# Performance work log

Hardware: AMD Instinct MI355X
Metric: run time of the kernel (lower is better)

The kernel has to match this reference:

```python
import jax, jax.numpy as jnp
import numpy as np

T, H, F = 4096, 4096, 14336

def setup_inputs() -> dict:
    key = jax.random.key(0)
    k1, k2, k3, k4 = jax.random.split(key, 4)
    s = 1.0 / np.sqrt(H)
    return {
        "x": jax.random.normal(k1, (T, H), dtype=jnp.float32),
        "expert_w1": jax.random.normal(k2, (H, F), dtype=jnp.float32) * s,
        "expert_v1": jax.random.normal(k3, (H, F), dtype=jnp.float32) * s,
        "expert_w2": jax.random.normal(k4, (H, F), dtype=jnp.float32) * s,
    }

def reference(x, expert_w1, expert_v1, expert_w2):
    # SwiGLU expert FFN: silu(x @ w1) * (x @ v1) @ w2.T
    gate_proj = jax.nn.silu(x @ expert_w1)          # [T, F]
    up_proj = x @ expert_v1                          # [T, F]
    down_proj = (gate_proj * up_proj) @ expert_w2.T  # [T, H]
    return down_proj
```

## Files before the change

kernel.cpp:

```cpp
#include <hip/hip_runtime.h>
#include <hip/hip_bf16.h>
#include <stdint.h>

#define TT 4096
#define HH 4096
#define FF 14336
#define NCAT (2 * FF)

typedef __attribute__((ext_vector_type(8))) short bf16x8;
typedef __attribute__((ext_vector_type(4))) float f32x4;

__device__ __forceinline__ unsigned short f32_to_bf16(float f) {
    union { float f; unsigned int u; } v; v.f = f;
    unsigned int r = v.u + 0x7FFFu + ((v.u >> 16) & 1u);
    return (unsigned short)(r >> 16);
}

#define GLOAD16(g, l)                                                          \
    __builtin_amdgcn_global_load_lds(                                          \
        (const __attribute__((address_space(1))) void*)(g),                    \
        (__attribute__((address_space(3))) void*)(l), 16, 0, 0)

__global__ void cvt_lin(const float* __restrict__ in,
                        unsigned short* __restrict__ out, long n4) {
    long stride = (long)gridDim.x * blockDim.x;
    for (long i = (long)blockIdx.x * blockDim.x + threadIdx.x; i < n4; i += stride) {
        float4 v = *(const float4*)(in + i * 4);
        ushort4 o;
        o.x = f32_to_bf16(v.x); o.y = f32_to_bf16(v.y);
        o.z = f32_to_bf16(v.z); o.w = f32_to_bf16(v.w);
        *(ushort4*)(out + i * 4) = o;
    }
}

__global__ void cvt_tri(const float* __restrict__ in,
                        unsigned short* __restrict__ out, int off) {
    __shared__ float tile[64][65];
    int bh = blockIdx.x & 63;
    int bf = blockIdx.x >> 6;
    int t = threadIdx.x;
    int r16 = t >> 4;
    int c4 = (t & 15) * 4;
#pragma unroll
    for (int it = 0; it < 4; ++it) {
        int h = r16 + it * 16;
        float4 v = *(const float4*)(in + (size_t)(bh * 64 + h) * FF + bf * 64 + c4);
        tile[h][c4 + 0] = v.x; tile[h][c4 + 1] = v.y;
        tile[h][c4 + 2] = v.z; tile[h][c4 + 3] = v.w;
    }
    __syncthreads();
#pragma unroll
    for (int it = 0; it < 4; ++it) {
        int f = r16 + it * 16;
        int fg = bf * 64 + f;
        int row_out = ((fg >> 4) << 5) + (fg & 15) + off;
        ushort4 o;
        o.x = f32_to_bf16(tile[c4 + 0][f]);
        o.y = f32_to_bf16(tile[c4 + 1][f]);
        o.z = f32_to_bf16(tile[c4 + 2][f]);
        o.w = f32_to_bf16(tile[c4 + 3][f]);
        *(ushort4*)(out + (size_t)row_out * HH + bh * 64 + c4) = o;
    }
}


#define STG_A(BUF, SLOT, TILE) do {                                            \
    char* d_ = lsA + (((BUF)*2 + (SLOT)) << 14) + tid * 16;                    \
    GLOAD16(sA[SLOT][0] + (size_t)(TILE) * 64, d_);                            \
    GLOAD16(sA[SLOT][1] + (size_t)(TILE) * 64, d_ + 8192);                     \
  } while (0)

#define STG_B(BUF, SLOT, TILE) do {                                            \
    char* d_ = lsB + (((BUF)*2 + (SLOT)) << 14) + tid * 16;                    \
    GLOAD16(sB[SLOT][0] + (size_t)(TILE) * 64, d_);                            \
    GLOAD16(sB[SLOT][1] + (size_t)(TILE) * 64, d_ + 8192);                     \
  } while (0)

#define READ_A(DST, BUF, MQ) do {                                              \
    const char* pA_ = lsA + (((BUF)*2 + (MQ)) << 14);                          \
    _Pragma("unroll") for (int i_ = 0; i_ < 4; ++i_)                           \
    _Pragma("unroll") for (int k_ = 0; k_ < 2; ++k_)                           \
      DST[i_][k_] = *(const bf16x8*)(pA_ + ((((wr*64 + i_*16 + fr) << 7) + k_*64 + kg2) ^ lmask)); \
  } while (0)

#define READ_B(DST, BUF, NQ) do {                                              \
    const char* pB_ = lsB + (((BUF)*2 + (NQ)) << 14);                          \
    _Pragma("unroll") for (int j_ = 0; j_ < 2; ++j_)                           \
    _Pragma("unroll") for (int k_ = 0; k_ < 2; ++k_)                           \
      DST[j_][k_] = *(const bf16x8*)(pB_ + ((((wc*32 + j_*16 + fr) << 7) + k_*64 + kg2) ^ lmask)); \
  } while (0)

#define MFMA_Q(MQ, NQ, AF, BF)                                                 \
    _Pragma("unroll") for (int i_ = 0; i_ < 4; ++i_)                           \
    _Pragma("unroll") for (int j_ = 0; j_ < 2; ++j_)                           \
    _Pragma("unroll") for (int k_ = 0; k_ < 2; ++k_)                           \
      acc[MQ][i_][NQ][j_] = __builtin_amdgcn_mfma_f32_16x16x32_bf16(           \
          AF[i_][k_], BF[j_][k_], acc[MQ][i_][NQ][j_], 0, 0, 0)

#define BAR do {                                                               \
    asm volatile("" ::: "memory");                                             \
    __builtin_amdgcn_s_barrier();                                              \
    asm volatile("" ::: "memory");                                             \
  } while (0)

#define VMC8 asm volatile("s_waitcnt vmcnt(8)" ::: "memory")
#define VMC0 asm volatile("s_waitcnt vmcnt(0)" ::: "memory")

#define PH(READS, STAGES, MQ, NQ, AF, BF, FENCE) do {                          \
    READS;                                                                     \
    STAGES;                                                                    \
    BAR;                                                                       \
    __builtin_amdgcn_s_setprio(1);                                             \
    MFMA_Q(MQ, NQ, AF, BF);                                                    \
    __builtin_amdgcn_s_setprio(0);                                             \
    FENCE;                                                                     \
    BAR;                                                                       \
  } while (0)

#define HALF_STG(BUF, TS, F4)                                                  \
    PH(READ_A(af, BUF, 0); READ_B(bf0, BUF, 0), , 0, 0, af, bf0, );            \
    PH(READ_B(bf1, BUF, 1), STG_A(BUF, 0, TS); STG_B(BUF, 0, TS), 0, 1, af, bf1, ); \
    PH(READ_A(af, BUF, 1), STG_B(BUF, 1, TS), 1, 1, af, bf1, );                \
    PH(, STG_A(BUF, 1, TS), 1, 0, af, bf0, F4);

#define HALF_NOSTG(BUF, F4)                                                    \
    PH(READ_A(af, BUF, 0); READ_B(bf0, BUF, 0), , 0, 0, af, bf0, );            \
    PH(READ_B(bf1, BUF, 1), , 0, 1, af, bf1, );                                \
    PH(READ_A(af, BUF, 1), , 1, 1, af, bf1, );                                 \
    PH(, , 1, 0, af, bf0, F4);

#define GEMM8_CORE(A_, LDA_, B_, LDB_, NT_)                                    \
  extern __shared__ char smem[];                                               \
  char* const lsA = smem;                                                      \
  char* const lsB = smem + 65536;                                              \
  const int tid = threadIdx.x;                                                 \
  const int lane = tid & 63;                                                   \
  const int wid = tid >> 6;                                                    \
  const int wr = wid >> 2;                                                     \
  const int wc = wid & 3;                                                      \
  const int fr = lane & 15;                                                    \
  const int kg2 = ((lane >> 4) & 3) << 4;                                      \
  const int lmask = (fr & 6) << 4;                                             \
  f32x4 acc[2][4][2][2];                                                       \
  _Pragma("unroll") for (int a_ = 0; a_ < 2; ++a_)                             \
  _Pragma("unroll") for (int b_ = 0; b_ < 4; ++b_)                             \
  _Pragma("unroll") for (int c_ = 0; c_ < 2; ++c_)                             \
  _Pragma("unroll") for (int d_ = 0; d_ < 2; ++d_)                             \
    acc[a_][b_][c_][d_] = (f32x4){0.f, 0.f, 0.f, 0.f};                         \
  bf16x8 af[4][2], bf0[2][2], bf1[2][2];                                       \
  const unsigned short* sA[2][2];                                              \
  const unsigned short* sB[2][2];                                              \
  _Pragma("unroll") for (int c_ = 0; c_ < 2; ++c_) {                           \
    int d_ = (tid + 512 * c_) * 16;                                            \
    int p_ = d_ ^ (((d_ >> 8) & 3) << 5);                                      \
    int prow = p_ >> 7, pcol = (p_ & 127) >> 1;                                \
    _Pragma("unroll") for (int s_ = 0; s_ < 2; ++s_) {                         \
      int grA = m0 + ((prow >> 6) & 1) * 128 + s_ * 64 + (prow & 63);          \
      sA[s_][c_] = (A_) + (size_t)grA * (LDA_) + pcol;                         \
      int grB = n0 + (prow >> 5) * 64 + s_ * 32 + (prow & 31);                 \
      sB[s_][c_] = (B_) + (size_t)grB * (LDB_) + pcol;                         \
    }                                                                          \
  }                                                                            \
        \
  STG_A(0, 0, 0); STG_B(0, 0, 0); STG_A(0, 1, 0); STG_B(0, 1, 0);              \
  STG_A(1, 0, 1); STG_B(1, 0, 1); STG_A(1, 1, 1); STG_B(1, 1, 1);              \
  VMC8;                                                                        \
  __builtin_amdgcn_s_barrier();                                                \
  asm volatile("" ::: "memory");                                               \
  const int niter = (NT_) / 2;                                                 \
  for (int I = 0; I < niter - 1; ++I) {                                        \
    const int t = 2 * I;                                                       \
    HALF_STG(0, t + 2, VMC8)                                                   \
    HALF_STG(1, t + 3, VMC8)                                                   \
  }                                                                            \
  HALF_NOSTG(0, VMC0)                                                          \
  HALF_NOSTG(1, )

__global__ __launch_bounds__(512)
__attribute__((amdgpu_waves_per_eu(1, 2))) void gemm_swiglu(
    const unsigned short* __restrict__ Xb,
    const unsigned short* __restrict__ Wcat,
    unsigned short* __restrict__ Act) {
    const int NWG = (TT / 256) * (NCAT / 256);
    int lid = (blockIdx.x & 7) * (NWG / 8) + (blockIdx.x >> 3);
    const int m0 = (lid & 15) * 256;
    const int n0 = (lid >> 4) * 256;

    GEMM8_CORE(Xb, HH, Wcat, HH, HH / 64)

    const int dm = ((lane >> 4) & 3) * 4;
    const int dn = lane & 15;
#pragma unroll
    for (int mq = 0; mq < 2; ++mq)
#pragma unroll
        for (int i = 0; i < 4; ++i)
#pragma unroll
            for (int nq = 0; nq < 2; ++nq) {
                int rowb = m0 + wr * 128 + mq * 64 + i * 16 + dm;
                int col = (n0 + wc * 64 + nq * 32) / 2 + dn;
                f32x4 g4 = acc[mq][i][nq][0];
                f32x4 u4 = acc[mq][i][nq][1];
#pragma unroll
                for (int r = 0; r < 4; ++r) {
                    float g = g4[r], u = u4[r];
                    float s = g * u / (1.0f + __expf(-g));
                    Act[(size_t)(rowb + r) * FF + col] = f32_to_bf16(s);
                }
            }
}

__global__ __launch_bounds__(512)
__attribute__((amdgpu_waves_per_eu(1, 2))) void gemm_down(
    const unsigned short* __restrict__ Act,
    const unsigned short* __restrict__ W2b,
    float* __restrict__ Out) {
    const int NWG = (TT / 256) * (HH / 256);
    int lid = (blockIdx.x & 7) * (NWG / 8) + (blockIdx.x >> 3);
    const int m0 = (lid & 15) * 256;
    const int n0 = (lid >> 4) * 256;

    GEMM8_CORE(Act, FF, W2b, FF, FF / 64)

    const int dm = ((lane >> 4) & 3) * 4;
    const int dn = lane & 15;
#pragma unroll
    for (int mq = 0; mq < 2; ++mq)
#pragma unroll
        for (int i = 0; i < 4; ++i)
#pragma unroll
            for (int nq = 0; nq < 2; ++nq)
#pragma unroll
                for (int j = 0; j < 2; ++j) {
                    int rowb = m0 + wr * 128 + mq * 64 + i * 16 + dm;
                    int col = n0 + wc * 64 + nq * 32 + j * 16 + dn;
                    f32x4 v = acc[mq][i][nq][j];
#pragma unroll
                    for (int r = 0; r < 4; ++r)
                        Out[(size_t)(rowb + r) * HH + col] = v[r];
                }
}

extern "C" void kernel_launch(void* const* d_in, const int* in_sizes, int n_in,
                              void* d_out, int out_size, void* d_ws, size_t ws_size,
                              hipStream_t stream) {
    const float* x  = (const float*)d_in[0];
    const float* w1 = (const float*)d_in[1];
    const float* v1 = (const float*)d_in[2];
    const float* w2 = (const float*)d_in[3];
    float* out = (float*)d_out;

    unsigned short* xb   = (unsigned short*)d_ws;
    unsigned short* wcat = xb + (size_t)TT * HH;
    unsigned short* w2b  = wcat + (size_t)NCAT * HH;
    unsigned short* act  = w2b + (size_t)HH * FF;

    hipFuncSetAttribute((const void*)gemm_swiglu,
                        hipFuncAttributeMaxDynamicSharedMemorySize, 131072);
    hipFuncSetAttribute((const void*)gemm_down,
                        hipFuncAttributeMaxDynamicSharedMemorySize, 131072);

    cvt_lin<<<2048, 256, 0, stream>>>(x, xb, (long)TT * HH / 4);
    cvt_lin<<<2048, 256, 0, stream>>>(w2, w2b, (long)HH * FF / 4);
    cvt_tri<<<(HH / 64) * (FF / 64), 256, 0, stream>>>(w1, wcat, 0);
    cvt_tri<<<(HH / 64) * (FF / 64), 256, 0, stream>>>(v1, wcat, 16);

    gemm_swiglu<<<(TT / 256) * (NCAT / 256), 512, 131072, stream>>>(xb, wcat, act);
    gemm_down<<<(TT / 256) * (HH / 256), 512, 131072, stream>>>(act, w2b, out);
}
```

Measured before the change: 1.587 ms.

## Reschedule LDS staging so B quarter of next tile issues one phase earlier

Reorders the global-to-LDS staging within the 8-wave GEMM pipeline. One B sub-tile of the next k-tile is now staged into the other buffer a phase earlier, and the last phase re-reads B fragments. The wait counter changes from vmcnt(8) to vmcnt(6) to match. The goal is to spread memory traffic more evenly across phases and cut stalls at the buffer-swap barrier. The cost is tighter buffer-hazard reasoning, where a wrong ordering could read stale LDS.

New measurement: 1.373 ms. 1.16x faster.

```diff
diff --git a/kernel.cpp b/kernel.cpp
--- a/kernel.cpp
+++ b/kernel.cpp
@@ -103,7 +103,7 @@
     asm volatile("" ::: "memory");                                             \
   } while (0)
 
-#define VMC8 asm volatile("s_waitcnt vmcnt(8)" ::: "memory")
+#define VMC6 asm volatile("s_waitcnt vmcnt(6)" ::: "memory")
 #define VMC0 asm volatile("s_waitcnt vmcnt(0)" ::: "memory")
 
 #define PH(READS, STAGES, MQ, NQ, AF, BF, FENCE) do {                          \
@@ -117,17 +117,23 @@
     BAR;                                                                       \
   } while (0)
 
-#define HALF_STG(BUF, TS, F4)                                                  \
-    PH(READ_A(af, BUF, 0); READ_B(bf0, BUF, 0), , 0, 0, af, bf0, );            \
-    PH(READ_B(bf1, BUF, 1), STG_A(BUF, 0, TS); STG_B(BUF, 0, TS), 0, 1, af, bf1, ); \
-    PH(READ_A(af, BUF, 1), STG_B(BUF, 1, TS), 1, 1, af, bf1, );                \
-    PH(, STG_A(BUF, 1, TS), 1, 0, af, bf0, F4);
-
-#define HALF_NOSTG(BUF, F4)                                                    \
+#define HALF_STG(BUF, OB, T)                                                   \
+    PH(READ_A(af, BUF, 0); READ_B(bf0, BUF, 0), STG_B(OB, 0, (T) + 1), 0, 0, af, bf0, ); \
+    PH(READ_B(bf1, BUF, 1), STG_A(BUF, 0, (T) + 2), 0, 1, af, bf1, );          \
+    PH(READ_A(af, BUF, 1), , 1, 1, af, bf1, );                                 \
+    PH(READ_B(bf0, BUF, 0), STG_B(BUF, 1, (T) + 2); STG_A(BUF, 1, (T) + 2), 1, 0, af, bf0, VMC6);
+
+#define HALF_T1(BUF, OB, T)                                                    \
+    PH(READ_A(af, BUF, 0); READ_B(bf0, BUF, 0), STG_B(OB, 0, (T) + 1), 0, 0, af, bf0, ); \
+    PH(READ_B(bf1, BUF, 1), , 0, 1, af, bf1, );                                \
+    PH(READ_A(af, BUF, 1), , 1, 1, af, bf1, );                                 \
+    PH(READ_B(bf0, BUF, 0), , 1, 0, af, bf0, VMC0);
+
+#define HALF_T2(BUF)                                                           \
     PH(READ_A(af, BUF, 0); READ_B(bf0, BUF, 0), , 0, 0, af, bf0, );            \
     PH(READ_B(bf1, BUF, 1), , 0, 1, af, bf1, );                                \
     PH(READ_A(af, BUF, 1), , 1, 1, af, bf1, );                                 \
-    PH(, , 1, 0, af, bf0, F4);
+    PH(READ_B(bf0, BUF, 0), , 1, 0, af, bf0, );
 
 #define GEMM8_CORE(A_, LDA_, B_, LDB_, NT_)                                    \
   extern __shared__ char smem[];                                               \
@@ -161,20 +167,21 @@
       sB[s_][c_] = (B_) + (size_t)grB * (LDB_) + pcol;                         \
     }                                                                          \
   }                                                                            \
-        \
-  STG_A(0, 0, 0); STG_B(0, 0, 0); STG_A(0, 1, 0); STG_B(0, 1, 0);              \
-  STG_A(1, 0, 1); STG_B(1, 0, 1); STG_A(1, 1, 1); STG_B(1, 1, 1);              \
-  VMC8;                                                                        \
+     \
+               \
+  STG_A(0, 0, 0); STG_B(0, 0, 0); STG_B(0, 1, 0); STG_A(0, 1, 0);              \
+  STG_A(1, 0, 1); STG_B(1, 1, 1); STG_A(1, 1, 1);                              \
+  VMC6;                                                                        \
   __builtin_amdgcn_s_barrier();                                                \
   asm volatile("" ::: "memory");                                               \
   const int niter = (NT_) / 2;                                                 \
   for (int I = 0; I < niter - 1; ++I) {                                        \
     const int t = 2 * I;                                                       \
-    HALF_STG(0, t + 2, VMC8)                                                   \
-    HALF_STG(1, t + 3, VMC8)                                                   \
+    HALF_STG(0, 1, t)                                                          \
+    HALF_STG(1, 0, t + 1)                                                      \
   }                                                                            \
-  HALF_NOSTG(0, VMC0)                                                          \
-  HALF_NOSTG(1, )
+  HALF_T1(0, 1, (NT_) - 2)                                                     \
+  HALF_T2(1)
 
 __global__ __launch_bounds__(512)
 __attribute__((amdgpu_waves_per_eu(1, 2))) void gemm_swiglu(
```

## Drop mid-phase barrier, prefetch next B fragment early, use 32-bit global offsets

Applied to the files above, without the earlier changes.

Removes the barrier between the LDS reads/stage issue and the MFMA block in each phase, leaving one barrier per phase. The first B fragment of the next buffer is now read at the end of the previous half, after the vmcnt wait, so it overlaps with the barrier instead of starting the next phase. Global source pointers are replaced by 32-bit byte offsets from a base to save VGPRs and address arithmetic, and the order of the B and A stage issues is swapped. This risks LDS hazards without the extra barrier and relies on offsets fitting in 32 bits.

Measured after the change: 1.300 ms. 1.22x faster.

```diff
diff --git a/kernel.cpp b/kernel.cpp
--- a/kernel.cpp
+++ b/kernel.cpp
@@ -64,27 +64,27 @@
 }
 
 
-#define STG_A(BUF, SLOT, TILE) do {                                            \
-    char* d_ = lsA + (((BUF)*2 + (SLOT)) << 14) + tid * 16;                    \
-    GLOAD16(sA[SLOT][0] + (size_t)(TILE) * 64, d_);                            \
-    GLOAD16(sA[SLOT][1] + (size_t)(TILE) * 64, d_ + 8192);                     \
-  } while (0)
-
-#define STG_B(BUF, SLOT, TILE) do {                                            \
-    char* d_ = lsB + (((BUF)*2 + (SLOT)) << 14) + tid * 16;                    \
-    GLOAD16(sB[SLOT][0] + (size_t)(TILE) * 64, d_);                            \
-    GLOAD16(sB[SLOT][1] + (size_t)(TILE) * 64, d_ + 8192);                     \
+#define STG_A(BUF, SLOT, T) do {                                               \
+    char* d_ = (char*)smem + (((BUF)*2 + (SLOT)) << 14) + tid * 16;            \
+    GLOAD16(Abase + (size_t)(oA[SLOT][0] + (unsigned)(T) * 128), d_);          \
+    GLOAD16(Abase + (size_t)(oA[SLOT][1] + (unsigned)(T) * 128), d_ + 8192);   \
+  } while (0)
+
+#define STG_B(BUF, SLOT, T) do {                                               \
+    char* d_ = (char*)smem + 65536 + (((BUF)*2 + (SLOT)) << 14) + tid * 16;    \
+    GLOAD16(Bbase + (size_t)(oB[SLOT][0] + (unsigned)(T) * 128), d_);          \
+    GLOAD16(Bbase + (size_t)(oB[SLOT][1] + (unsigned)(T) * 128), d_ + 8192);   \
   } while (0)
 
 #define READ_A(DST, BUF, MQ) do {                                              \
-    const char* pA_ = lsA + (((BUF)*2 + (MQ)) << 14);                          \
+    const char* pA_ = (const char*)smem + (((BUF)*2 + (MQ)) << 14);            \
     _Pragma("unroll") for (int i_ = 0; i_ < 4; ++i_)                           \
     _Pragma("unroll") for (int k_ = 0; k_ < 2; ++k_)                           \
       DST[i_][k_] = *(const bf16x8*)(pA_ + ((((wr*64 + i_*16 + fr) << 7) + k_*64 + kg2) ^ lmask)); \
   } while (0)
 
 #define READ_B(DST, BUF, NQ) do {                                              \
-    const char* pB_ = lsB + (((BUF)*2 + (NQ)) << 14);                          \
+    const char* pB_ = (const char*)smem + 65536 + (((BUF)*2 + (NQ)) << 14);    \
     _Pragma("unroll") for (int j_ = 0; j_ < 2; ++j_)                           \
     _Pragma("unroll") for (int k_ = 0; k_ < 2; ++k_)                           \
       DST[j_][k_] = *(const bf16x8*)(pB_ + ((((wc*32 + j_*16 + fr) << 7) + k_*64 + kg2) ^ lmask)); \
@@ -106,33 +106,42 @@
 #define VMC8 asm volatile("s_waitcnt vmcnt(8)" ::: "memory")
 #define VMC0 asm volatile("s_waitcnt vmcnt(0)" ::: "memory")
 
-#define PH(READS, STAGES, MQ, NQ, AF, BF, FENCE) do {                          \
+#define PHX(READS, STAGES, MQ, NQ, AF, BF, FENCE, POST) do {                   \
     READS;                                                                     \
     STAGES;                                                                    \
-    BAR;                                                                       \
     __builtin_amdgcn_s_setprio(1);                                             \
     MFMA_Q(MQ, NQ, AF, BF);                                                    \
     __builtin_amdgcn_s_setprio(0);                                             \
     FENCE;                                                                     \
+    POST;                                                                      \
     BAR;                                                                       \
   } while (0)
 
-#define HALF_STG(BUF, TS, F4)                                                  \
-    PH(READ_A(af, BUF, 0); READ_B(bf0, BUF, 0), , 0, 0, af, bf0, );            \
-    PH(READ_B(bf1, BUF, 1), STG_A(BUF, 0, TS); STG_B(BUF, 0, TS), 0, 1, af, bf1, ); \
-    PH(READ_A(af, BUF, 1), STG_B(BUF, 1, TS), 1, 1, af, bf1, );                \
-    PH(, STG_A(BUF, 1, TS), 1, 0, af, bf0, F4);
-
-#define HALF_NOSTG(BUF, F4)                                                    \
-    PH(READ_A(af, BUF, 0); READ_B(bf0, BUF, 0), , 0, 0, af, bf0, );            \
-    PH(READ_B(bf1, BUF, 1), , 0, 1, af, bf1, );                                \
-    PH(READ_A(af, BUF, 1), , 1, 1, af, bf1, );                                 \
-    PH(, , 1, 0, af, bf0, F4);
+#define PH(READS, STAGES, MQ, NQ, AF, BF, FENCE)                               \
+    PHX(READS, STAGES, MQ, NQ, AF, BF, FENCE, )
+
+#define HALF_STG(BUF, OB, TS)                                                  \
+    PH(READ_A(af, BUF, 0), , 0, 0, af, bfA, );                                 \
+    PH(READ_B(bfB, BUF, 1), STG_A(BUF, 0, TS); STG_B(BUF, 0, TS), 0, 1, af, bfB, ); \
+    PH(READ_A(af, BUF, 1), STG_B(BUF, 1, TS), 1, 1, af, bfB, );                \
+    PHX(, STG_A(BUF, 1, TS), 1, 0, af, bfA, VMC8, READ_B(bfA, OB, 0));
+
+#define HALF_T1(BUF, OB)                                                       \
+    PH(READ_A(af, BUF, 0), , 0, 0, af, bfA, );                                 \
+    PH(READ_B(bfB, BUF, 1), , 0, 1, af, bfB, );                                \
+    PH(READ_A(af, BUF, 1), , 1, 1, af, bfB, );                                 \
+    PHX(, , 1, 0, af, bfA, VMC0, READ_B(bfA, OB, 0));
+
+#define HALF_T2(BUF)                                                           \
+    PH(READ_A(af, BUF, 0), , 0, 0, af, bfA, );                                 \
+    PH(READ_B(bfB, BUF, 1), , 0, 1, af, bfB, );                                \
+    PH(READ_A(af, BUF, 1), , 1, 1, af, bfB, );                                 \
+    PHX(, , 1, 0, af, bfA, , );
 
 #define GEMM8_CORE(A_, LDA_, B_, LDB_, NT_)                                    \
   extern __shared__ char smem[];                                               \
-  char* const lsA = smem;                                                      \
-  char* const lsB = smem + 65536;                                              \
+  const char* const Abase = (const char*)(A_);                                 \
+  const char* const Bbase = (const char*)(B_);                                 \
   const int tid = threadIdx.x;                                                 \
   const int lane = tid & 63;                                                   \
   const int wid = tid >> 6;                                                    \
@@ -147,34 +156,33 @@
   _Pragma("unroll") for (int c_ = 0; c_ < 2; ++c_)                             \
   _Pragma("unroll") for (int d_ = 0; d_ < 2; ++d_)                             \
     acc[a_][b_][c_][d_] = (f32x4){0.f, 0.f, 0.f, 0.f};                         \
-  bf16x8 af[4][2], bf0[2][2], bf1[2][2];                                       \
-  const unsigned short* sA[2][2];                                              \
-  const unsigned short* sB[2][2];                                              \
+  bf16x8 af[4][2], bfA[2][2], bfB[2][2];                                       \
+  unsigned int oA[2][2], oB[2][2];                                             \
   _Pragma("unroll") for (int c_ = 0; c_ < 2; ++c_) {                           \
     int d_ = (tid + 512 * c_) * 16;                                            \
     int p_ = d_ ^ (((d_ >> 8) & 3) << 5);                                      \
     int prow = p_ >> 7, pcol = (p_ & 127) >> 1;                                \
     _Pragma("unroll") for (int s_ = 0; s_ < 2; ++s_) {                         \
       int grA = m0 + ((prow >> 6) & 1) * 128 + s_ * 64 + (prow & 63);          \
-      sA[s_][c_] = (A_) + (size_t)grA * (LDA_) + pcol;                         \
+      oA[s_][c_] = (unsigned)((size_t)grA * (LDA_) + pcol) * 2u;               \
       int grB = n0 + (prow >> 5) * 64 + s_ * 32 + (prow & 31);                 \
-      sB[s_][c_] = (B_) + (size_t)grB * (LDB_) + pcol;                         \
+      oB[s_][c_] = (unsigned)((size_t)grB * (LDB_) + pcol) * 2u;               \
     }                                                                          \
   }                                                                            \
-        \
-  STG_A(0, 0, 0); STG_B(0, 0, 0); STG_A(0, 1, 0); STG_B(0, 1, 0);              \
-  STG_A(1, 0, 1); STG_B(1, 0, 1); STG_A(1, 1, 1); STG_B(1, 1, 1);              \
+     \
+  STG_A(0, 0, 0); STG_B(0, 0, 0); STG_B(0, 1, 0); STG_A(0, 1, 0);              \
+  STG_A(1, 0, 1); STG_B(1, 0, 1); STG_B(1, 1, 1); STG_A(1, 1, 1);              \
   VMC8;                                                                        \
   __builtin_amdgcn_s_barrier();                                                \
   asm volatile("" ::: "memory");                                               \
+  READ_B(bfA, 0, 0);                                                           \
   const int niter = (NT_) / 2;                                                 \
   for (int I = 0; I < niter - 1; ++I) {                                        \
-    const int t = 2 * I;                                                       \
-    HALF_STG(0, t + 2, VMC8)                                                   \
-    HALF_STG(1, t + 3, VMC8)                                                   \
+    HALF_STG(0, 1, 2 * I + 2)                                                  \
+    HALF_STG(1, 0, 2 * I + 3)                                                  \
   }                                                                            \
-  HALF_NOSTG(0, VMC0)                                                          \
-  HALF_NOSTG(1, )
+  HALF_T1(0, 1)                                                                \
+  HALF_T2(1)
 
 __global__ __launch_bounds__(512)
 __attribute__((amdgpu_waves_per_eu(1, 2))) void gemm_swiglu(
```
